# Performance work log

Hardware: AMD Instinct MI355X
Metric: run time of the kernel (lower is better)

Reference implementation:

```python
import jax, jax.numpy as jnp
import numpy as np

X_DIM, H_DIM, SEQ, BATCH = 38, 128, 128, 2048


def _gru_step(h, x_t, Wih, Whh, bih, bhh):
    # PyTorch GRUCell: gates ordered (r, z, n)
    gi = x_t @ Wih.T + bih          # [B, 3H]
    gh = h @ Whh.T + bhh            # [B, 3H]
    gi_r, gi_z, gi_n = jnp.split(gi, 3, axis=-1)
    gh_r, gh_z, gh_n = jnp.split(gh, 3, axis=-1)
    r = jax.nn.sigmoid(gi_r + gh_r)
    z = jax.nn.sigmoid(gi_z + gh_z)
    n = jnp.tanh(gi_n + r * gh_n)
    return (1.0 - z) * n + z * h


def setup_inputs() -> dict:
    key = jax.random.key(0)
    ks = jax.random.split(key, 12)
    s_x = 1.0 / np.sqrt(H_DIM)
    inp = {
        "x": jax.random.normal(ks[0], (BATCH, SEQ, X_DIM), dtype=jnp.float32),
        "enc_Wih": jax.random.uniform(ks[1], (3 * H_DIM, X_DIM), minval=-s_x, maxval=s_x, dtype=jnp.float32),
        "enc_Whh": jax.random.uniform(ks[2], (3 * H_DIM, H_DIM), minval=-s_x, maxval=s_x, dtype=jnp.float32),
        "enc_bih": jax.random.uniform(ks[3], (3 * H_DIM,), minval=-s_x, maxval=s_x, dtype=jnp.float32),
        "enc_bhh": jax.random.uniform(ks[4], (3 * H_DIM,), minval=-s_x, maxval=s_x, dtype=jnp.float32),
        "dec_Wih": jax.random.uniform(ks[5], (3 * H_DIM, X_DIM), minval=-s_x, maxval=s_x, dtype=jnp.float32),
        "dec_Whh": jax.random.uniform(ks[6], (3 * H_DIM, H_DIM), minval=-s_x, maxval=s_x, dtype=jnp.float32),
        "dec_bih": jax.random.uniform(ks[7], (3 * H_DIM,), minval=-s_x, maxval=s_x, dtype=jnp.float32),
        "dec_bhh": jax.random.uniform(ks[8], (3 * H_DIM,), minval=-s_x, maxval=s_x, dtype=jnp.float32),
        "lin_W": jax.random.uniform(ks[9], (X_DIM, H_DIM), minval=-s_x, maxval=s_x, dtype=jnp.float32),
        "lin_b": jax.random.uniform(ks[10], (X_DIM,), minval=-s_x, maxval=s_x, dtype=jnp.float32),
    }
    return inp


def reference(x, enc_Wih, enc_Whh, enc_bih, enc_bhh,
              dec_Wih, dec_Whh, dec_bih, dec_bhh, lin_W, lin_b):
    B, T, _ = x.shape
    H = enc_Whh.shape[1]
    X = x.shape[-1]
    xs = jnp.swapaxes(x, 0, 1)  # [T, B, X]

    # Encoder: scan GRUCell over time, h0 = zeros
    def enc_step(h, x_t):
        h = _gru_step(h, x_t, enc_Wih, enc_Whh, enc_bih, enc_bhh)
        return h, None
    h0 = jnp.zeros((B, H), dtype=x.dtype)
    h_enc, _ = jax.lax.scan(enc_step, h0, xs)

    def dec_step(carry, _):
        h, o_prev = carry
        h = _gru_step(h, o_prev, dec_Wih, dec_Whh, dec_bih, dec_bhh)
        o = h @ lin_W.T + lin_b  # [B, X]
        return (h, o), o
    go = jnp.zeros((B, X), dtype=x.dtype)
    _, outs = jax.lax.scan(dec_step, (h_enc, go), None, length=T)  # [T, B, X]
    return jnp.swapaxes(outs, 0, 1)  # [B, T, X]
```

## Files before the change

kernel.cpp:

```cpp
#include <hip/hip_runtime.h>
#include <cstdint>


#define T_SEQ 128
#define X_DIM 38
#define H_DIM 128
#define B_TOT 2048
#define BT    8
#define HS    136
#define XK    40
#define XCH   64

#define HB_BYTES   (2 * BT * HS * 2)
#define XC_BYTES   (XCH * BT * XK * 2)
#define SMEM_BYTES (HB_BYTES + XC_BYTES)

typedef _Float16 half8 __attribute__((ext_vector_type(8)));
typedef float    f32x4 __attribute__((ext_vector_type(4)));

#define MF(a, b, c) __builtin_amdgcn_mfma_f32_16x16x32_f16((a), (b), (c), 0, 0, 0)

__device__ __forceinline__ float fast_sigmoid(float x) {
    return __builtin_amdgcn_rcpf(1.0f + __expf(-x));
}
__device__ __forceinline__ float fast_tanh(float x) {
    return 1.0f - 2.0f * __builtin_amdgcn_rcpf(1.0f + __expf(2.0f * x));
}

#define ENC_STEP(HRD, HWR, TLOC)                                               \
    do {                                                                       \
        const _Float16* xr_ = xchunk + ((TLOC) * BT + arow) * XK;              \
        half8 xa0_ = *(const half8*)(xr_ + quad * 8);                          \
        half8 xa1_ = xa0_;              \
        if (quad == 0) xa1_ = *(const half8*)(xr_ + 32);                       \
        const _Float16* hb_ = (HRD) + arow * HS + quad * 8;                    \
        half8 h0_ = *(const half8*)(hb_ + 0 * 32);                             \
        half8 h1_ = *(const half8*)(hb_ + 1 * 32);                             \
        half8 h2_ = *(const half8*)(hb_ + 2 * 32);                             \
        half8 h3_ = *(const half8*)(hb_ + 3 * 32);                             \
        f32x4 ar_ = { b_r, b_r, b_r, b_r };                                    \
        ar_ = MF(xa0_, wxe[0][0], ar_);                                        \
        ar_ = MF(xa1_, wxe[0][1], ar_);                                        \
        ar_ = MF(h0_, wh[0][0], ar_);                                          \
        f32x4 arB_ = { 0.f, 0.f, 0.f, 0.f };                                   \
        arB_ = MF(h1_, wh[0][1], arB_);                                        \
        arB_ = MF(h2_, wh[0][2], arB_);                                        \
        arB_ = MF(h3_, wh[0][3], arB_);                                        \
        f32x4 az_ = { b_z, b_z, b_z, b_z };                                    \
        az_ = MF(xa0_, wxe[1][0], az_);                                        \
        az_ = MF(xa1_, wxe[1][1], az_);                                        \
        az_ = MF(h0_, wh[1][0], az_);                                          \
        f32x4 azB_ = { 0.f, 0.f, 0.f, 0.f };                                   \
        azB_ = MF(h1_, wh[1][1], azB_);                                        \
        azB_ = MF(h2_, wh[1][2], azB_);                                        \
        azB_ = MF(h3_, wh[1][3], azB_);                                        \
        f32x4 gin_ = { b_ngi, b_ngi, b_ngi, b_ngi };                           \
        gin_ = MF(xa0_, wxe[2][0], gin_);                                      \
        gin_ = MF(xa1_, wxe[2][1], gin_);                                      \
        f32x4 gn_ = { b_ngh, b_ngh, b_ngh, b_ngh };                            \
        gn_ = MF(h0_, wh[2][0], gn_);                                          \
        gn_ = MF(h1_, wh[2][1], gn_);                                          \
        f32x4 gnB_ = { 0.f, 0.f, 0.f, 0.f };                                   \
        gnB_ = MF(h2_, wh[2][2], gnB_);                                        \
        gnB_ = MF(h3_, wh[2][3], gnB_);                                        \
        _Pragma("unroll")                                                      \
        for (int e_ = 0; e_ < 2; ++e_) {                                       \
            const int rg_ = 2 * e_;           \
            const float r_ = fast_sigmoid(ar_[rg_] + arB_[rg_]);               \
            const float z_ = fast_sigmoid(az_[rg_] + azB_[rg_]);               \
            const float n_ = fast_tanh(gin_[rg_] + r_ * (gn_[rg_] + gnB_[rg_]));\
            const float h_ = n_ + z_ * (hold[e_] - n_);                        \
            hold[e_] = h_;                                                     \
            (HWR)[(2 * quad + e_) * HS + j] = (_Float16)h_;                    \
        }                                                                      \
        __syncthreads();                                                       \
    } while (0)

#define DEC_STEP(HRD, HWR, TOUT)                                               \
    do {                                                                       \
        const _Float16* hb_ = (HRD) + arow * HS + quad * 8;                    \
        half8 h0_ = *(const half8*)(hb_ + 0 * 32);                             \
        half8 h1_ = *(const half8*)(hb_ + 1 * 32);                             \
        half8 h2_ = *(const half8*)(hb_ + 2 * 32);                             \
        half8 h3_ = *(const half8*)(hb_ + 3 * 32);                             \
        if (wv < 3) {   \
            f32x4 al_ = { lb, lb, lb, lb };                                    \
            al_ = MF(h0_, wl[0], al_);                                         \
            al_ = MF(h1_, wl[1], al_);                                         \
            f32x4 alB_ = { 0.f, 0.f, 0.f, 0.f };                               \
            alB_ = MF(h2_, wl[2], alB_);                                       \
            alB_ = MF(h3_, wl[3], alB_);                                       \
            if (nv) {                                                          \
                out[obase0 + (size_t)(TOUT) * X_DIM] = al_[0] + alB_[0];       \
                out[obase1 + (size_t)(TOUT) * X_DIM] = al_[2] + alB_[2];       \
            }                                                                  \
        }                                                                      \
        f32x4 ar_ = { b_r, b_r, b_r, b_r };                                    \
        ar_ = MF(h0_, wh[0][0], ar_);                                          \
        ar_ = MF(h1_, wh[0][1], ar_);                                          \
        f32x4 arB_ = { 0.f, 0.f, 0.f, 0.f };                                   \
        arB_ = MF(h2_, wh[0][2], arB_);                                        \
        arB_ = MF(h3_, wh[0][3], arB_);                                        \
        f32x4 az_ = { b_z, b_z, b_z, b_z };                                    \
        az_ = MF(h0_, wh[1][0], az_);                                          \
        az_ = MF(h1_, wh[1][1], az_);                                          \
        f32x4 azB_ = { 0.f, 0.f, 0.f, 0.f };                                   \
        azB_ = MF(h2_, wh[1][2], azB_);                                        \
        azB_ = MF(h3_, wh[1][3], azB_);                                        \
        f32x4 gn_ = { b_ngh, b_ngh, b_ngh, b_ngh };                            \
        gn_ = MF(h0_, wh[2][0], gn_);                                          \
        gn_ = MF(h1_, wh[2][1], gn_);                                          \
        f32x4 gnB_ = { 0.f, 0.f, 0.f, 0.f };                                   \
        gnB_ = MF(h2_, wh[2][2], gnB_);                                        \
        gnB_ = MF(h3_, wh[2][3], gnB_);                                        \
        f32x4 gi_ = { b_ngi, b_ngi, b_ngi, b_ngi };                            \
        gi_ = MF(h0_, wxn[0], gi_);                                            \
        gi_ = MF(h1_, wxn[1], gi_);                                            \
        f32x4 giB_ = { 0.f, 0.f, 0.f, 0.f };                                   \
        giB_ = MF(h2_, wxn[2], giB_);                                          \
        giB_ = MF(h3_, wxn[3], giB_);                                          \
        _Pragma("unroll")                                                      \
        for (int e_ = 0; e_ < 2; ++e_) {                                       \
            const int rg_ = 2 * e_;                                            \
            const float r_ = fast_sigmoid(ar_[rg_] + arB_[rg_]);               \
            const float z_ = fast_sigmoid(az_[rg_] + azB_[rg_]);               \
            const float n_ = fast_tanh((gi_[rg_] + giB_[rg_]) +                \
                                       r_ * (gn_[rg_] + gnB_[rg_]));           \
            const float h_ = n_ + z_ * (hold[e_] - n_);                        \
            hold[e_] = h_;                                                     \
            (HWR)[(2 * quad + e_) * HS + j] = (_Float16)h_;                    \
        }                                                                      \
        __syncthreads();                                                       \
    } while (0)

__global__ __launch_bounds__(512, 2)
void rae_gru_kernel(const float* __restrict__ x,
                    const float* __restrict__ eWih, const float* __restrict__ eWhh,
                    const float* __restrict__ ebih, const float* __restrict__ ebhh,
                    const float* __restrict__ dWih, const float* __restrict__ dWhh,
                    const float* __restrict__ dbih, const float* __restrict__ dbhh,
                    const float* __restrict__ linW, const float* __restrict__ linb,
                    float* __restrict__ out)
{
    __shared__ __align__(16) unsigned char smem[SMEM_BYTES];
    _Float16* const hbuf0  = (_Float16*)smem;
    _Float16* const hbuf1  = hbuf0 + BT * HS;
    _Float16* const xchunk = (_Float16*)(smem + HB_BYTES);
    _Float16* const w2lds  = xchunk;

    const int tid  = threadIdx.x;
    const int wv   = tid >> 6;
    const int ln   = tid & 63;
    const int quad = ln >> 4;
    const int mrow = ln & 15;
    const int b0   = blockIdx.x * BT;
    const int arow = mrow >> 1;
    const int j    = wv * 16 + mrow;
    const int jc0  = j, jc1 = H_DIM + j, jc2 = 2 * H_DIM + j;

    {
        uint32_t* hz = (uint32_t*)smem;
        #pragma unroll
        for (int i = tid; i < HB_BYTES / 4; i += 512) hz[i] = 0u;
    }

    auto stage_x = [&](int tb) {
        const int st = tid & 63, sr = tid >> 6;
        const float* src = x + ((size_t)(b0 + sr) * T_SEQ + tb + st) * X_DIM;
        _Float16* dst = xchunk + ((size_t)st * BT + sr) * XK;
        float v[38];
        #pragma unroll
        for (int u = 0; u < 19; ++u) {
            float2 w = *(const float2*)(src + 2 * u);
            v[2 * u] = w.x; v[2 * u + 1] = w.y;
        }
        #pragma unroll
        for (int c = 0; c < 4; ++c) {
            half8 hv;
            #pragma unroll
            for (int e = 0; e < 8; ++e) hv[e] = (_Float16)v[c * 8 + e];
            *(half8*)(dst + c * 8) = hv;
        }
        {
            half8 hv;
            #pragma unroll
            for (int e = 0; e < 6; ++e) hv[e] = (_Float16)v[32 + e];
            hv[6] = (_Float16)0.0f; hv[7] = (_Float16)0.0f;
            *(half8*)(dst + 32) = hv;
        }
    };
    stage_x(0);

    half8 wh[3][4];
    half8 wxe[3][2];
    half8 wxn[4];
    half8 wl[4];
    float b_r, b_z, b_ngi, b_ngh;

    #pragma unroll
    for (int p = 0; p < 3; ++p) {
        const int jp = p * H_DIM + j;
        const float* wr = eWhh + (size_t)jp * H_DIM;
        #pragma unroll
        for (int c = 0; c < 4; ++c) {
            const int kb = c * 32 + quad * 8;
            half8 v;
            #pragma unroll
            for (int e = 0; e < 8; ++e) v[e] = (_Float16)wr[kb + e];
            wh[p][c] = v;
        }
        const float* wir = eWih + (size_t)jp * X_DIM;
        #pragma unroll
        for (int c = 0; c < 2; ++c) {
            const int kb = c * 32 + quad * 8;
            half8 v;
            #pragma unroll
            for (int e = 0; e < 8; ++e) {
                const int k = kb + e;
                v[e] = (k < X_DIM) ? (_Float16)wir[k] : (_Float16)0.0f;
            }
            wxe[p][c] = v;
        }
    }
    b_r   = ebih[jc0] + ebhh[jc0];
    b_z   = ebih[jc1] + ebhh[jc1];
    b_ngi = ebih[jc2];
    b_ngh = ebhh[jc2];

    float hold[2] = { 0.0f, 0.0f };

    __syncthreads();

    #pragma unroll 1
    for (int i = 0; i < 32; ++i) {
        ENC_STEP(hbuf0, hbuf1, 2 * i);
        ENC_STEP(hbuf1, hbuf0, 2 * i + 1);
    }
    stage_x(XCH);
    __syncthreads();
    #pragma unroll 1
    for (int i = 0; i < 32; ++i) {
        ENC_STEP(hbuf0, hbuf1, 2 * i);
        ENC_STEP(hbuf1, hbuf0, 2 * i + 1);
    }

    #pragma unroll
    for (int p = 0; p < 3; ++p) {
        const float* wr = dWhh + (size_t)(p * H_DIM + j) * H_DIM;
        #pragma unroll
        for (int c = 0; c < 4; ++c) {
            const int kb = c * 32 + quad * 8;
            half8 v;
            #pragma unroll
            for (int e = 0; e < 8; ++e) v[e] = (_Float16)wr[kb + e];
            wh[p][c] = v;
        }
    }
    const float c_r0 = dbih[jc0] + dbhh[jc0];
    const float c_z0 = dbih[jc1] + dbhh[jc1];
    const float c_n0 = dbih[jc2];
    b_ngh = dbhh[jc2];

    {
        const _Float16* hb_ = hbuf0 + arow * HS + quad * 8;
        half8 h0_ = *(const half8*)(hb_ + 0 * 32);
        half8 h1_ = *(const half8*)(hb_ + 1 * 32);
        half8 h2_ = *(const half8*)(hb_ + 2 * 32);
        half8 h3_ = *(const half8*)(hb_ + 3 * 32);
        f32x4 ar_ = { c_r0, c_r0, c_r0, c_r0 };
        ar_ = MF(h0_, wh[0][0], ar_);
        ar_ = MF(h1_, wh[0][1], ar_);
        f32x4 arB_ = { 0.f, 0.f, 0.f, 0.f };
        arB_ = MF(h2_, wh[0][2], arB_);
        arB_ = MF(h3_, wh[0][3], arB_);
        f32x4 az_ = { c_z0, c_z0, c_z0, c_z0 };
        az_ = MF(h0_, wh[1][0], az_);
        az_ = MF(h1_, wh[1][1], az_);
        f32x4 azB_ = { 0.f, 0.f, 0.f, 0.f };
        azB_ = MF(h2_, wh[1][2], azB_);
        azB_ = MF(h3_, wh[1][3], azB_);
        f32x4 gn_ = { b_ngh, b_ngh, b_ngh, b_ngh };
        gn_ = MF(h0_, wh[2][0], gn_);
        gn_ = MF(h1_, wh[2][1], gn_);
        f32x4 gnB_ = { 0.f, 0.f, 0.f, 0.f };
        gnB_ = MF(h2_, wh[2][2], gnB_);
        gnB_ = MF(h3_, wh[2][3], gnB_);
        #pragma unroll
        for (int e_ = 0; e_ < 2; ++e_) {
            const int rg_ = 2 * e_;
            const float r_ = fast_sigmoid(ar_[rg_] + arB_[rg_]);
            const float z_ = fast_sigmoid(az_[rg_] + azB_[rg_]);
            const float n_ = fast_tanh(c_n0 + r_ * (gn_[rg_] + gnB_[rg_]));
            const float h_ = n_ + z_ * (hold[e_] - n_);
            hold[e_] = h_;
            hbuf1[(2 * quad + e_) * HS + j] = (_Float16)h_;
        }
    }
    __syncthreads();

    {
        const int kk = ((wv & 1) << 6) | ln;
        const int jb = (wv >> 1) * 32;
        float lc[X_DIM];
        #pragma unroll
        for (int m = 0; m < X_DIM; ++m) lc[m] = linW[m * H_DIM + kk];

        #pragma unroll 1
        for (int jj = 0; jj < 32; ++jj) {
            const int jr = __builtin_amdgcn_readfirstlane(jb + jj);
            const float* dwr = dWih + (size_t)jr * X_DIM;
            float sacc = dWhh[(size_t)jr * H_DIM + kk];
            #pragma unroll
            for (int m = 0; m < X_DIM; ++m) sacc += dwr[m] * lc[m];
            w2lds[jr * H_DIM + kk] = (_Float16)sacc;
        }
        __syncthreads();
        #pragma unroll
        for (int c = 0; c < 4; ++c)
            wh[0][c] = *(const half8*)&w2lds[j * H_DIM + c * 32 + quad * 8];
        __syncthreads();

        #pragma unroll 1
        for (int jj = 0; jj < 32; ++jj) {
            const int jr = __builtin_amdgcn_readfirstlane(jb + jj);
            const float* dwr = dWih + (size_t)(H_DIM + jr) * X_DIM;
            float sacc = dWhh[(size_t)(H_DIM + jr) * H_DIM + kk];
            #pragma unroll
            for (int m = 0; m < X_DIM; ++m) sacc += dwr[m] * lc[m];
            w2lds[jr * H_DIM + kk] = (_Float16)sacc;
        }
        __syncthreads();
        #pragma unroll
        for (int c = 0; c < 4; ++c)
            wh[1][c] = *(const half8*)&w2lds[j * H_DIM + c * 32 + quad * 8];
        __syncthreads();

        #pragma unroll 1
        for (int jj = 0; jj < 32; ++jj) {
            const int jr = __builtin_amdgcn_readfirstlane(jb + jj);
            const float* dwr = dWih + (size_t)(2 * H_DIM + jr) * X_DIM;
            float sacc = 0.0f;
            #pragma unroll
            for (int m = 0; m < X_DIM; ++m) sacc += dwr[m] * lc[m];
            w2lds[jr * H_DIM + kk] = (_Float16)sacc;
        }
        __syncthreads();
        #pragma unroll
        for (int c = 0; c < 4; ++c)
            wxn[c] = *(const half8*)&w2lds[j * H_DIM + c * 32 + quad * 8];
        __syncthreads();
    }

    const int nlin = wv * 16 + mrow;
    const bool nv = (wv < 3) && (nlin < X_DIM);
    float lb = 0.0f;
    {
        const float* lr = linW + (size_t)(nv ? nlin : 0) * H_DIM;
        #pragma unroll
        for (int c = 0; c < 4; ++c) {
            const int kb = c * 32 + quad * 8;
            half8 v;
            #pragma unroll
            for (int e = 0; e < 8; ++e)
                v[e] = nv ? (_Float16)lr[kb + e] : (_Float16)0.0f;
            wl[c] = v;
        }
        if (nv) lb = linb[nlin];
    }
    {
        float bf[3];
        #pragma unroll
        for (int p = 0; p < 3; ++p) {
            const float* dwr = dWih + (size_t)(p * H_DIM + j) * X_DIM;
            float sacc = 0.0f;
            #pragma unroll
            for (int m = 0; m < X_DIM; ++m) sacc += linb[m] * dwr[m];
            bf[p] = sacc;
        }
        b_r   = c_r0 + bf[0];
        b_z   = c_z0 + bf[1];
        b_ngi = c_n0 + bf[2];
    }

    const size_t obase0 = ((size_t)(b0 + 2 * quad)     * T_SEQ) * X_DIM + nlin;
    const size_t obase1 = ((size_t)(b0 + 2 * quad + 1) * T_SEQ) * X_DIM + nlin;

    #pragma unroll 1
    for (int i = 0; i < 63; ++i) {
        DEC_STEP(hbuf1, hbuf0, 2 * i);
        DEC_STEP(hbuf0, hbuf1, 2 * i + 1);
    }
    DEC_STEP(hbuf1, hbuf0, 126);

    if (wv < 3) {
        const _Float16* hb_ = hbuf0 + arow * HS + quad * 8;
        half8 h0_ = *(const half8*)(hb_ + 0 * 32);
        half8 h1_ = *(const half8*)(hb_ + 1 * 32);
        half8 h2_ = *(const half8*)(hb_ + 2 * 32);
        half8 h3_ = *(const half8*)(hb_ + 3 * 32);
        f32x4 al_ = { lb, lb, lb, lb };
        al_ = MF(h0_, wl[0], al_);
        al_ = MF(h1_, wl[1], al_);
        f32x4 alB_ = { 0.f, 0.f, 0.f, 0.f };
        alB_ = MF(h2_, wl[2], alB_);
        alB_ = MF(h3_, wl[3], alB_);
        if (nv) {
            out[obase0 + (size_t)(T_SEQ - 1) * X_DIM] = al_[0] + alB_[0];
            out[obase1 + (size_t)(T_SEQ - 1) * X_DIM] = al_[2] + alB_[2];
        }
    }
}

extern "C" void kernel_launch(void* const* d_in, const int* in_sizes, int n_in,
                              void* d_out, int out_size, void* d_ws, size_t ws_size,
                              hipStream_t stream) {
    (void)in_sizes; (void)n_in; (void)d_ws; (void)ws_size; (void)out_size;
    const float* x    = (const float*)d_in[0];
    const float* eWih = (const float*)d_in[1];
    const float* eWhh = (const float*)d_in[2];
    const float* ebih = (const float*)d_in[3];
    const float* ebhh = (const float*)d_in[4];
    const float* dWih = (const float*)d_in[5];
    const float* dWhh = (const float*)d_in[6];
    const float* dbih = (const float*)d_in[7];
    const float* dbhh = (const float*)d_in[8];
    const float* linW = (const float*)d_in[9];
    const float* linb = (const float*)d_in[10];
    float* out = (float*)d_out;

    rae_gru_kernel<<<dim3(B_TOT / BT), dim3(512), 0, stream>>>(
        x, eWih, eWhh, ebih, ebhh, dWih, dWhh, dbih, dbhh, linW, linb, out);
}
```

Measured before the change: 297.5 us.

## Precompute next-step encoder input gate MFMAs off the recurrent critical path

```diff
diff --git a/kernel.cpp b/kernel.cpp
--- a/kernel.cpp
+++ b/kernel.cpp
@@ -12,7 +12,7 @@
 #define XCH   64
 
 #define HB_BYTES   (2 * BT * HS * 2)
-#define XC_BYTES   (XCH * BT * XK * 2)
+#define XC_BYTES   ((XCH + 1) * BT * XK * 2)
 #define SMEM_BYTES (HB_BYTES + XC_BYTES)
 
 typedef _Float16 half8 __attribute__((ext_vector_type(8)));
@@ -27,52 +27,57 @@
     return 1.0f - 2.0f * __builtin_amdgcn_rcpf(1.0f + __expf(2.0f * x));
 }
 
-#define ENC_STEP(HRD, HWR, TLOC)                                               \
+#define XG_CALC(TLOC, OUTr, OUTz, OUTn)                                        \
     do {                                                                       \
         const _Float16* xr_ = xchunk + ((TLOC) * BT + arow) * XK;              \
-        half8 xa0_ = *(const half8*)(xr_ + quad * 8);                          \
-        half8 xa1_ = xa0_;              \
-        if (quad == 0) xa1_ = *(const half8*)(xr_ + 32);                       \
+        half8 x0_ = *(const half8*)(xr_ + quad * 8);                           \
+        half8 x1_ = *(const half8*)(xr_ + 32);                                 \
+        OUTr = MF(x0_, wxe[0][0], vb_r);                                       \
+        OUTr = MF(x1_, wxe[0][1], OUTr);                                       \
+        OUTz = MF(x0_, wxe[1][0], vb_z);                                       \
+        OUTz = MF(x1_, wxe[1][1], OUTz);                                       \
+        OUTn = MF(x0_, wxe[2][0], vb_ngi);                                     \
+        OUTn = MF(x1_, wxe[2][1], OUTn);                                       \
+    } while (0)
+
+#define ENC_STEP(HRD, HWR, TLOC, INr, INz, INn, OUTr, OUTz, OUTn)              \
+    do {                                                                       \
+        const _Float16* xn_ = xchunk + (((TLOC) + 1) * BT + arow) * XK;        \
+        half8 xn0_ = *(const half8*)(xn_ + quad * 8);                          \
+        half8 xn1_ = *(const half8*)(xn_ + 32);                                \
         const _Float16* hb_ = (HRD) + arow * HS + quad * 8;                    \
         half8 h0_ = *(const half8*)(hb_ + 0 * 32);                             \
         half8 h1_ = *(const half8*)(hb_ + 1 * 32);                             \
         half8 h2_ = *(const half8*)(hb_ + 2 * 32);                             \
         half8 h3_ = *(const half8*)(hb_ + 3 * 32);                             \
-        f32x4 ar_ = { b_r, b_r, b_r, b_r };                                    \
-        ar_ = MF(xa0_, wxe[0][0], ar_);                                        \
-        ar_ = MF(xa1_, wxe[0][1], ar_);                                        \
-        ar_ = MF(h0_, wh[0][0], ar_);                                          \
-        f32x4 arB_ = { 0.f, 0.f, 0.f, 0.f };                                   \
-        arB_ = MF(h1_, wh[0][1], arB_);                                        \
-        arB_ = MF(h2_, wh[0][2], arB_);                                        \
+        f32x4 ar_ = MF(h0_, wh[0][0], INr);                                    \
+        ar_ = MF(h1_, wh[0][1], ar_);                                          \
+        f32x4 arB_ = MF(h2_, wh[0][2], vzero);                                 \
         arB_ = MF(h3_, wh[0][3], arB_);                                        \
-        f32x4 az_ = { b_z, b_z, b_z, b_z };                                    \
-        az_ = MF(xa0_, wxe[1][0], az_);                                        \
-        az_ = MF(xa1_, wxe[1][1], az_);                                        \
-        az_ = MF(h0_, wh[1][0], az_);                                          \
-        f32x4 azB_ = { 0.f, 0.f, 0.f, 0.f };                                   \
-        azB_ = MF(h1_, wh[1][1], azB_);                                        \
-        azB_ = MF(h2_, wh[1][2], azB_);                                        \
+        f32x4 az_ = MF(h0_, wh[1][0], INz);                                    \
+        az_ = MF(h1_, wh[1][1], az_);                                          \
+        f32x4 azB_ = MF(h2_, wh[1][2], vzero);                                 \
         azB_ = MF(h3_, wh[1][3], azB_);                                        \
-        f32x4 gin_ = { b_ngi, b_ngi, b_ngi, b_ngi };                           \
-        gin_ = MF(xa0_, wxe[2][0], gin_);                                      \
-        gin_ = MF(xa1_, wxe[2][1], gin_);                                      \
-        f32x4 gn_ = { b_ngh, b_ngh, b_ngh, b_ngh };                            \
-        gn_ = MF(h0_, wh[2][0], gn_);                                          \
+        f32x4 gn_ = MF(h0_, wh[2][0], vb_ngh);                                 \
         gn_ = MF(h1_, wh[2][1], gn_);                                          \
-        f32x4 gnB_ = { 0.f, 0.f, 0.f, 0.f };                                   \
-        gnB_ = MF(h2_, wh[2][2], gnB_);                                        \
+        f32x4 gnB_ = MF(h2_, wh[2][2], vzero);                                 \
         gnB_ = MF(h3_, wh[2][3], gnB_);                                        \
         _Pragma("unroll")                                                      \
         for (int e_ = 0; e_ < 2; ++e_) {                                       \
             const int rg_ = 2 * e_;           \
             const float r_ = fast_sigmoid(ar_[rg_] + arB_[rg_]);               \
             const float z_ = fast_sigmoid(az_[rg_] + azB_[rg_]);               \
-            const float n_ = fast_tanh(gin_[rg_] + r_ * (gn_[rg_] + gnB_[rg_]));\
+            const float n_ = fast_tanh(INn[rg_] + r_ * (gn_[rg_] + gnB_[rg_]));\
             const float h_ = n_ + z_ * (hold[e_] - n_);                        \
             hold[e_] = h_;                                                     \
             (HWR)[(2 * quad + e_) * HS + j] = (_Float16)h_;                    \
         }                                                                      \
+        OUTr = MF(xn0_, wxe[0][0], vb_r);           \
+        OUTr = MF(xn1_, wxe[0][1], OUTr);           \
+        OUTz = MF(xn0_, wxe[1][0], vb_z);                                      \
+        OUTz = MF(xn1_, wxe[1][1], OUTz);                                      \
+        OUTn = MF(xn0_, wxe[2][0], vb_ngi);                                    \
+        OUTn = MF(xn1_, wxe[2][1], OUTn);                                      \
         __syncthreads();                                                       \
     } while (0)
 
@@ -83,41 +88,31 @@
         half8 h1_ = *(const half8*)(hb_ + 1 * 32);                             \
         half8 h2_ = *(const half8*)(hb_ + 2 * 32);                             \
         half8 h3_ = *(const half8*)(hb_ + 3 * 32);                             \
-        if (wv < 3) {   \
-            f32x4 al_ = { lb, lb, lb, lb };                                    \
-            al_ = MF(h0_, wl[0], al_);                                         \
+        if (wv < 3) {             \
+            f32x4 al_ = MF(h0_, wl[0], vb_lb);                                 \
             al_ = MF(h1_, wl[1], al_);                                         \
-            f32x4 alB_ = { 0.f, 0.f, 0.f, 0.f };                               \
-            alB_ = MF(h2_, wl[2], alB_);                                       \
+            f32x4 alB_ = MF(h2_, wl[2], vzero);                                \
             alB_ = MF(h3_, wl[3], alB_);                                       \
             if (nv) {                                                          \
                 out[obase0 + (size_t)(TOUT) * X_DIM] = al_[0] + alB_[0];       \
                 out[obase1 + (size_t)(TOUT) * X_DIM] = al_[2] + alB_[2];       \
             }                                                                  \
         }                                                                      \
-        f32x4 ar_ = { b_r, b_r, b_r, b_r };                                    \
-        ar_ = MF(h0_, wh[0][0], ar_);                                          \
+        f32x4 ar_ = MF(h0_, wh[0][0], vd_r);                                   \
         ar_ = MF(h1_, wh[0][1], ar_);                                          \
-        f32x4 arB_ = { 0.f, 0.f, 0.f, 0.f };                                   \
-        arB_ = MF(h2_, wh[0][2], arB_);                                        \
+        f32x4 arB_ = MF(h2_, wh[0][2], vzero);                                 \
         arB_ = MF(h3_, wh[0][3], arB_);                                        \
-        f32x4 az_ = { b_z, b_z, b_z, b_z };                                    \
-        az_ = MF(h0_, wh[1][0], az_);                                          \
+        f32x4 az_ = MF(h0_, wh[1][0], vd_z);                                   \
         az_ = MF(h1_, wh[1][1], az_);                                          \
-        f32x4 azB_ = { 0.f, 0.f, 0.f, 0.f };                                   \
-        azB_ = MF(h2_, wh[1][2], azB_);                                        \
+        f32x4 azB_ = MF(h2_, wh[1][2], vzero);                                 \
         azB_ = MF(h3_, wh[1][3], azB_);                                        \
-        f32x4 gn_ = { b_ngh, b_ngh, b_ngh, b_ngh };                            \
-        gn_ = MF(h0_, wh[2][0], gn_);                                          \
+        f32x4 gn_ = MF(h0_, wh[2][0], vd_gh);                                  \
         gn_ = MF(h1_, wh[2][1], gn_);                                          \
-        f32x4 gnB_ = { 0.f, 0.f, 0.f, 0.f };                                   \
-        gnB_ = MF(h2_, wh[2][2], gnB_);                                        \
+        f32x4 gnB_ = MF(h2_, wh[2][2], vzero);                                 \
         gnB_ = MF(h3_, wh[2][3], gnB_);                                        \
-        f32x4 gi_ = { b_ngi, b_ngi, b_ngi, b_ngi };                            \
-        gi_ = MF(h0_, wxn[0], gi_);                                            \
+        f32x4 gi_ = MF(h0_, wxn[0], vd_gi);                                    \
         gi_ = MF(h1_, wxn[1], gi_);                                            \
-        f32x4 giB_ = { 0.f, 0.f, 0.f, 0.f };                                   \
-        giB_ = MF(h2_, wxn[2], giB_);                                          \
+        f32x4 giB_ = MF(h2_, wxn[2], vzero);                                   \
         giB_ = MF(h3_, wxn[3], giB_);                                          \
         _Pragma("unroll")                                                      \
         for (int e_ = 0; e_ < 2; ++e_) {                                       \
@@ -160,8 +155,8 @@
 
     {
         uint32_t* hz = (uint32_t*)smem;
-        #pragma unroll
-        for (int i = tid; i < HB_BYTES / 4; i += 512) hz[i] = 0u;
+        #pragma unroll 1
+        for (int i = tid; i < SMEM_BYTES / 4; i += 512) hz[i] = 0u;
     }
 
     auto stage_x = [&](int tb) {
@@ -195,7 +190,7 @@
     half8 wxe[3][2];
     half8 wxn[4];
     half8 wl[4];
-    float b_r, b_z, b_ngi, b_ngh;
+    const f32x4 vzero = { 0.f, 0.f, 0.f, 0.f };
 
     #pragma unroll
     for (int p = 0; p < 3; ++p) {
@@ -222,26 +217,32 @@
             wxe[p][c] = v;
         }
     }
-    b_r   = ebih[jc0] + ebhh[jc0];
-    b_z   = ebih[jc1] + ebhh[jc1];
-    b_ngi = ebih[jc2];
-    b_ngh = ebhh[jc2];
+    const float eb_r   = ebih[jc0] + ebhh[jc0];
+    const float eb_z   = ebih[jc1] + ebhh[jc1];
+    const float eb_ngi = ebih[jc2];
+    const float eb_ngh = ebhh[jc2];
+    const f32x4 vb_r   = { eb_r, eb_r, eb_r, eb_r };
+    const f32x4 vb_z   = { eb_z, eb_z, eb_z, eb_z };
+    const f32x4 vb_ngi = { eb_ngi, eb_ngi, eb_ngi, eb_ngi };
+    const f32x4 vb_ngh = { eb_ngh, eb_ngh, eb_ngh, eb_ngh };
 
     float hold[2] = { 0.0f, 0.0f };
 
     __syncthreads();
 
+    f32x4 xgAr, xgAz, xgAn, xgBr, xgBz, xgBn;
     #pragma unroll 1
-    for (int i = 0; i < 32; ++i) {
-        ENC_STEP(hbuf0, hbuf1, 2 * i);
-        ENC_STEP(hbuf1, hbuf0, 2 * i + 1);
-    }
-    stage_x(XCH);
-    __syncthreads();
-    #pragma unroll 1
-    for (int i = 0; i < 32; ++i) {
-        ENC_STEP(hbuf0, hbuf1, 2 * i);
-        ENC_STEP(hbuf1, hbuf0, 2 * i + 1);
+    for (int ch = 0; ch < 2; ++ch) {
+        XG_CALC(0, xgAr, xgAz, xgAn);
+        #pragma unroll 1
+        for (int i = 0; i < 32; ++i) {
+            ENC_STEP(hbuf0, hbuf1, 2 * i,     xgAr, xgAz, xgAn, xgBr, xgBz, xgBn);
+            ENC_STEP(hbuf1, hbuf0, 2 * i + 1, xgBr, xgBz, xgBn, xgAr, xgAz, xgAn);
+        }
+        if (ch == 0) {
+            stage_x(XCH);
+            __syncthreads();
+        }
     }
 
     #pragma unroll
@@ -259,7 +260,8 @@
     const float c_r0 = dbih[jc0] + dbhh[jc0];
     const float c_z0 = dbih[jc1] + dbhh[jc1];
     const float c_n0 = dbih[jc2];
-    b_ngh = dbhh[jc2];
+    const float d_ngh = dbhh[jc2];
+    const f32x4 vd_gh = { d_ngh, d_ngh, d_ngh, d_ngh };
 
     {
         const _Float16* hb_ = hbuf0 + arow * HS + quad * 8;
@@ -270,20 +272,16 @@
         f32x4 ar_ = { c_r0, c_r0, c_r0, c_r0 };
         ar_ = MF(h0_, wh[0][0], ar_);
         ar_ = MF(h1_, wh[0][1], ar_);
-        f32x4 arB_ = { 0.f, 0.f, 0.f, 0.f };
-        arB_ = MF(h2_, wh[0][2], arB_);
+        f32x4 arB_ = MF(h2_, wh[0][2], vzero);
         arB_ = MF(h3_, wh[0][3], arB_);
         f32x4 az_ = { c_z0, c_z0, c_z0, c_z0 };
         az_ = MF(h0_, wh[1][0], az_);
         az_ = MF(h1_, wh[1][1], az_);
-        f32x4 azB_ = { 0.f, 0.f, 0.f, 0.f };
-        azB_ = MF(h2_, wh[1][2], azB_);
+        f32x4 azB_ = MF(h2_, wh[1][2], vzero);
         azB_ = MF(h3_, wh[1][3], azB_);
-        f32x4 gn_ = { b_ngh, b_ngh, b_ngh, b_ngh };
-        gn_ = MF(h0_, wh[2][0], gn_);
+        f32x4 gn_ = MF(h0_, wh[2][0], vd_gh);
         gn_ = MF(h1_, wh[2][1], gn_);
-        f32x4 gnB_ = { 0.f, 0.f, 0.f, 0.f };
-        gnB_ = MF(h2_, wh[2][2], gnB_);
+        f32x4 gnB_ = MF(h2_, wh[2][2], vzero);
         gnB_ = MF(h3_, wh[2][3], gnB_);
         #pragma unroll
         for (int e_ = 0; e_ < 2; ++e_) {
@@ -367,6 +365,7 @@
         }
         if (nv) lb = linb[nlin];
     }
+    float db_r, db_z, db_gi;
     {
         float bf[3];
         #pragma unroll
@@ -377,10 +376,14 @@
             for (int m = 0; m < X_DIM; ++m) sacc += linb[m] * dwr[m];
             bf[p] = sacc;
         }
-        b_r   = c_r0 + bf[0];
-        b_z   = c_z0 + bf[1];
-        b_ngi = c_n0 + bf[2];
-    }
+        db_r  = c_r0 + bf[0];
+        db_z  = c_z0 + bf[1];
+        db_gi = c_n0 + bf[2];
+    }
+    const f32x4 vd_r  = { db_r, db_r, db_r, db_r };
+    const f32x4 vd_z  = { db_z, db_z, db_z, db_z };
+    const f32x4 vd_gi = { db_gi, db_gi, db_gi, db_gi };
+    const f32x4 vb_lb = { lb, lb, lb, lb };
 
     const size_t obase0 = ((size_t)(b0 + 2 * quad)     * T_SEQ) * X_DIM + nlin;
     const size_t obase1 = ((size_t)(b0 + 2 * quad + 1) * T_SEQ) * X_DIM + nlin;
@@ -398,11 +401,9 @@
         half8 h1_ = *(const half8*)(hb_ + 1 * 32);
         half8 h2_ = *(const half8*)(hb_ + 2 * 32);
         half8 h3_ = *(const half8*)(hb_ + 3 * 32);
-        f32x4 al_ = { lb, lb, lb, lb };
-        al_ = MF(h0_, wl[0], al_);
+        f32x4 al_ = MF(h0_, wl[0], vb_lb);
         al_ = MF(h1_, wl[1], al_);
-        f32x4 alB_ = { 0.f, 0.f, 0.f, 0.f };
-        alB_ = MF(h2_, wl[2], alB_);
+        f32x4 alB_ = MF(h2_, wl[2], vzero);
         alB_ = MF(h3_, wl[3], alB_);
         if (nv) {
             out[obase0 + (size_t)(T_SEQ - 1) * X_DIM] = al_[0] + alB_[0];
```

After: 291.3 us. 2.1% less time.
